# Optimization experiments

Measured on AMD Instinct MI355X. Metric: run time of the kernel, lower is better.

## Reference

```python
import jax, jax.numpy as jnp
import numpy as np

B, S, E, H = 4, 1024, 768, 8
HD = E // H
FF = 4 * E
SCALING = HD ** -0.5


def _layernorm(x, g, b, eps=1e-5):
    m = jnp.mean(x, axis=-1, keepdims=True)
    v = jnp.var(x, axis=-1, keepdims=True)
    return (x - m) / jnp.sqrt(v + eps) * g + b


def setup_inputs() -> dict:
    key = jax.random.key(0)
    ks = jax.random.split(key, 12)
    w = lambda k, shp: (jax.random.normal(k, shp, jnp.float32) * 0.02)
    return {
        "x": jax.random.normal(ks[0], (B, S, E), jnp.float32),
        "dist_map": jax.random.uniform(ks[1], (B, H, S, S), jnp.float32),
        "mask": jnp.zeros((B, S), jnp.int32),
        "Wq": w(ks[2], (E, E)), "bq": jnp.zeros((E,), jnp.float32),
        "Wk": w(ks[3], (E, E)), "bk": jnp.zeros((E,), jnp.float32),
        "Wv": w(ks[4], (E, E)), "bv": jnp.zeros((E,), jnp.float32),
        "Wo": w(ks[5], (E, E)), "bo": jnp.zeros((E,), jnp.float32),
        "ln1_g": jnp.ones((E,), jnp.float32), "ln1_b": jnp.zeros((E,), jnp.float32),
        "W1": w(ks[6], (FF, E)), "b1": jnp.zeros((FF,), jnp.float32),
        "W2": w(ks[7], (E, FF)), "b2": jnp.zeros((E,), jnp.float32),
        "ln2_g": jnp.ones((E,), jnp.float32), "ln2_b": jnp.zeros((E,), jnp.float32),
    }


def reference(x, dist_map, mask, Wq, bq, Wk, bk, Wv, bv, Wo, bo,
              ln1_g, ln1_b, W1, b1, W2, b2, ln2_g, ln2_b):
    # --- attention residual block (pre-norm) ---
    h = _layernorm(x, ln1_g, ln1_b)
    # NOTE: torch does .view(B, H, S, HD) directly on [B, S, E] -> pure reshape, no transpose
    q = (h @ Wq.T + bq).reshape(B, H, S, HD)
    k = (h @ Wk.T + bk).reshape(B, H, S, HD)
    v = (h @ Wv.T + bv).reshape(B, H, S, HD)
    attn_weights = jnp.einsum("bhqd,bhkd->bhqk", q, k)
    pad = mask.astype(bool)[:, None, None, :]          # [B,1,1,S]
    attn_weights = jnp.where(pad, -10000.0, attn_weights)  # mask BEFORE scaling (as in source)
    probs = jax.nn.softmax(attn_weights * SCALING, axis=-1)
    probs = (probs + dist_map) * 0.5                   # post-softmax dist bias
    ctx = jnp.einsum("bhal,bhlv->bhav", probs, v)      # [B,H,S,HD]
    ctx = ctx.transpose(0, 2, 1, 3).reshape(B, S, E)
    x1 = x + (ctx @ Wo.T + bo)
    # --- FFN residual block (pre-norm) ---
    h2 = _layernorm(x1, ln2_g, ln2_b)
    ffn = jax.nn.gelu(h2 @ W1.T + b1, approximate=False) @ W2.T + b2
    out = x1 + ffn
    return out, probs
```

## Files before the change

### kernel.cpp

```cpp
#include <hip/hip_runtime.h>
#include <math.h>

typedef unsigned short u16;
typedef u16   u16x8  __attribute__((ext_vector_type(8)));
typedef u16   u16x4  __attribute__((ext_vector_type(4)));
typedef __bf16 bf16x8 __attribute__((ext_vector_type(8)));
typedef float f32x4  __attribute__((ext_vector_type(4)));

#define SZ_BSE   3145728
#define HEADSZ   98304
#define SCALING  0.10206207261596577f

__device__ __forceinline__ u16 f2bf(float f) {
  union { float f; unsigned u; } c; c.f = f;
  unsigned u = c.u;
  return (u16)((u + 0x7fffu + ((u >> 16) & 1u)) >> 16);
}

typedef const __attribute__((address_space(1))) unsigned int* gas1_t;
typedef __attribute__((address_space(3))) unsigned int* las3_t;
__device__ __forceinline__ void gload16(const void* g, void* l) {
  __builtin_amdgcn_global_load_lds((gas1_t)g, (las3_t)l, 16, 0, 0);
}

__global__ __launch_bounds__(256) void cvt_k(const float* __restrict__ in,
                                             u16* __restrict__ out, int n) {
  int i = (blockIdx.x * 256 + threadIdx.x) * 4;
  if (i >= n) return;
  f32x4 v = *(const f32x4*)&in[i];
  u16x4 o; o[0]=f2bf(v[0]); o[1]=f2bf(v[1]); o[2]=f2bf(v[2]); o[3]=f2bf(v[3]);
  *(u16x4*)&out[i] = o;
}

__global__ __launch_bounds__(256) void ln_k(const float* __restrict__ x,
                                            const float* __restrict__ g,
                                            const float* __restrict__ b,
                                            u16* __restrict__ out) {
  const int row = blockIdx.x;
  const float* xr = x + (long)row * 768;
  const int t = threadIdx.x;
  float v0 = xr[t], v1 = xr[t + 256], v2 = xr[t + 512];
  float s = v0 + v1 + v2, ss = v0*v0 + v1*v1 + v2*v2;
  for (int o = 32; o > 0; o >>= 1) { s += __shfl_xor(s, o); ss += __shfl_xor(ss, o); }
  __shared__ float red[8];
  int w = t >> 6;
  if ((t & 63) == 0) { red[w] = s; red[w + 4] = ss; }
  __syncthreads();
  s  = red[0] + red[1] + red[2] + red[3];
  ss = red[4] + red[5] + red[6] + red[7];
  float mean = s * (1.0f / 768.0f);
  float var  = ss * (1.0f / 768.0f) - mean * mean;
  float rstd = rsqrtf(var + 1e-5f);
  u16* orow = out + (long)row * 768;
  orow[t]       = f2bf((v0 - mean) * rstd * g[t]       + b[t]);
  orow[t + 256] = f2bf((v1 - mean) * rstd * g[t + 256] + b[t + 256]);
  orow[t + 512] = f2bf((v2 - mean) * rstd * g[t + 512] + b[t + 512]);
}

__global__ __launch_bounds__(256) void vtrans_k(const u16* __restrict__ v,
                                                u16* __restrict__ vt) {
  __shared__ u16 tile[64 * 98];
  const int z = blockIdx.x >> 4;
  const int s0 = (blockIdx.x & 15) << 6;
  const int t = threadIdx.x;
  const u16* src = v + (long)z * HEADSZ + (long)s0 * 96;
#pragma unroll
  for (int it = 0; it < 3; ++it) {
    int i = it * 2048 + t * 8;
    int s = i / 96, d = i % 96;
    *(u16x8*)&tile[s * 98 + d] = *(const u16x8*)&src[i];
  }
  __syncthreads();
  u16* dst = vt + (long)z * HEADSZ + s0;
#pragma unroll
  for (int it = 0; it < 6; ++it) {
    int o = it * 1024 + t * 4;
    int d = o >> 6, s = o & 63;
    u16x4 wv;
#pragma unroll
    for (int j = 0; j < 4; ++j) wv[j] = tile[(s + j) * 98 + d];
    *(u16x4*)&dst[(long)d * 1024 + s] = wv;
  }
}

__global__ __launch_bounds__(256) void reduce_k(const float* __restrict__ p,
                                                const float* __restrict__ resid,
                                                const float* __restrict__ bias,
                                                float* __restrict__ out) {
  long i = ((long)blockIdx.x * 256 + threadIdx.x) * 4;
  f32x4 a = *(const f32x4*)&p[i];
  f32x4 b = *(const f32x4*)&p[3145728 + i];
  f32x4 c = *(const f32x4*)&p[6291456 + i];
  f32x4 r = *(const f32x4*)&resid[i];
  int cb = (int)(i % 768);
  f32x4 g = *(const f32x4*)&bias[cb];
  f32x4 o;
  o[0] = r[0] + g[0] + a[0] + b[0] + c[0];
  o[1] = r[1] + g[1] + a[1] + b[1] + c[1];
  o[2] = r[2] + g[2] + a[2] + b[2] + c[2];
  o[3] = r[3] + g[3] + a[3] + b[3] + c[3];
  *(f32x4*)&out[i] = o;
}

__global__ __launch_bounds__(256, 2)
void attn_k(const u16* __restrict__ qb, const u16* __restrict__ kb,
            const u16* __restrict__ vT, const float* __restrict__ dist,
            const int* __restrict__ maskp, float* __restrict__ probs,
            u16* __restrict__ ctx) {
  __shared__ u16 sP[64 * 88];
  __shared__ u16 sFlag[1024];

  const int t = threadIdx.x;
  const int z = blockIdx.y;
  const int r0 = blockIdx.x * 64;
  const int b = z >> 3, h = z & 7;

  {
    const int* mp = maskp + b * 1024 + t * 4;
    int4 mv = *(const int4*)mp;
    sFlag[t*4+0] = (u16)(mv.x != 0);
    sFlag[t*4+1] = (u16)(mv.y != 0);
    sFlag[t*4+2] = (u16)(mv.z != 0);
    sFlag[t*4+3] = (u16)(mv.w != 0);
  }
  __syncthreads();

  const int lane = t & 63;
  const int w = t >> 6;
  const int wr0 = w * 16;
  const int lr = lane & 15;
  const int lg = lane >> 4;

  const u16* qh = qb + (long)z * HEADSZ;
  const u16* kh = kb + (long)z * HEADSZ;
  const u16* vh = vT + (long)z * HEADSZ;
  const float* dh = dist + (long)z * 1048576;
  float* ph = probs + (long)z * 1048576;

  bf16x8 qa[3];
  {
    const u16* qr = qh + (long)(r0 + wr0 + lr) * 96 + lg * 8;
#pragma unroll
    for (int kf = 0; kf < 3; ++kf) qa[kf] = *(const bf16x8*)(qr + kf * 32);
  }

  const float neg = -10000.0f * SCALING;
  float srun[4] = {0.f, 0.f, 0.f, 0.f};

  for (int c = 0; c < 16; ++c) {
    const int c0 = c * 64;
    f32x4 a4[4] = {};
#pragma unroll
    for (int ni = 0; ni < 4; ++ni) {
      const u16* kr = kh + (long)(c0 + ni * 16 + lr) * 96 + lg * 8;
#pragma unroll
      for (int kf = 0; kf < 3; ++kf)
        a4[ni] = __builtin_amdgcn_mfma_f32_16x16x32_bf16(
            qa[kf], *(const bf16x8*)(kr + kf * 32), a4[ni], 0, 0, 0);
    }
#pragma unroll
    for (int ni = 0; ni < 4; ++ni) {
      bool fm = sFlag[c0 + ni * 16 + lr] != 0;
#pragma unroll
      for (int r = 0; r < 4; ++r) {
        float sv = fm ? neg : a4[ni][r] * SCALING;
        srun[r] += __expf(sv);
      }
    }
  }
  float inv[4];
#pragma unroll
  for (int r = 0; r < 4; ++r) {
    float s = srun[r];
    s += __shfl_xor(s, 1);
    s += __shfl_xor(s, 2);
    s += __shfl_xor(s, 4);
    s += __shfl_xor(s, 8);
    inv[r] = 1.0f / s;
  }

  f32x4 cacc[6] = {};
  for (int c = 0; c < 16; ++c) {
    const int c0 = c * 64;
    f32x4 dv[4];
#pragma unroll
    for (int ni = 0; ni < 4; ++ni) {
      const float* dp = dh + (long)(r0 + wr0 + lg * 4) * 1024 + c0 + ni * 16 + lr;
#pragma unroll
      for (int r = 0; r < 4; ++r) dv[ni][r] = dp[r * 1024];
    }
    f32x4 a4[4] = {};
#pragma unroll
    for (int ni = 0; ni < 4; ++ni) {
      const u16* kr = kh + (long)(c0 + ni * 16 + lr) * 96 + lg * 8;
#pragma unroll
      for (int kf = 0; kf < 3; ++kf)
        a4[ni] = __builtin_amdgcn_mfma_f32_16x16x32_bf16(
            qa[kf], *(const bf16x8*)(kr + kf * 32), a4[ni], 0, 0, 0);
    }
#pragma unroll
    for (int ni = 0; ni < 4; ++ni) {
      bool fm = sFlag[c0 + ni * 16 + lr] != 0;
      float* pp = ph + (long)(r0 + wr0 + lg * 4) * 1024 + c0 + ni * 16 + lr;
      int sb = (wr0 + lg * 4) * 88 + ni * 16 + lr;
#pragma unroll
      for (int r = 0; r < 4; ++r) {
        float sv = fm ? neg : a4[ni][r] * SCALING;
        float e = __expf(sv) * inv[r];
        float pr = (e + dv[ni][r]) * 0.5f;
        pp[r * 1024] = pr;
        sP[sb + r * 88] = f2bf(pr);
      }
    }
#pragma unroll
    for (int ks = 0; ks < 2; ++ks) {
      bf16x8 pa = *(const bf16x8*)&sP[(wr0 + lr) * 88 + ks * 32 + lg * 8];
      const u16* vr = vh + (long)lr * 1024 + c0 + ks * 32 + lg * 8;
#pragma unroll
      for (int n2 = 0; n2 < 6; ++n2) {
        bf16x8 vb = *(const bf16x8*)(vr + (long)n2 * 16 * 1024);
        cacc[n2] = __builtin_amdgcn_mfma_f32_16x16x32_bf16(pa, vb, cacc[n2], 0, 0, 0);
      }
    }
  }

  u16* cbase = ctx + (long)b * 786432 + h * 96;
#pragma unroll
  for (int n2 = 0; n2 < 6; ++n2) {
    int d = n2 * 16 + lr;
#pragma unroll
    for (int r = 0; r < 4; ++r)
      cbase[(long)(r0 + wr0 + lg * 4 + r) * 768 + d] = f2bf(cacc[n2][r]);
  }
}

enum { EPI_QKV = 0, EPI_GELU = 1, EPI_PARTIAL = 2 };

template <int EPI>
__global__ __launch_bounds__(256, 2)
void gemm_k(const u16* __restrict__ A, int lda,
            const u16* __restrict__ W, int ldw,
            void* __restrict__ Cv, long sCz, int ldc,
            const float* __restrict__ bias,
            int N, int K, int kchunks) {
  __shared__ u16 sA[4096];
  __shared__ u16 sB[4096];

  const int t  = threadIdx.x;
  const int kc = blockIdx.z;
  const int klen = K / kchunks;
  const int kbeg = kc * klen, kend = kbeg + klen;
  const int m0 = blockIdx.x * 128;
  const int n0 = blockIdx.y * 128;

  const int r0 = t >> 2;
  const int c0 = (t & 3) << 3;
  char* lA = (char*)sA + ((t >> 6) << 10);
  char* lB = (char*)sB + ((t >> 6) << 10);

  int bn0 = n0 + r0;      if (bn0 > N - 1) bn0 = N - 1;
  int bn1 = n0 + 64 + r0; if (bn1 > N - 1) bn1 = N - 1;
  const u16* gB0 = W + (long)bn0 * ldw + c0;
  const u16* gB1 = W + (long)bn1 * ldw + c0;
  const u16* gA0 = A + (long)(m0 + r0) * lda + c0;
  const u16* gA1 = gA0 + 64 * lda;

  const int lane = t & 63;
  const int w  = t >> 6;
  const int wm = (w >> 1) * 64, wn = (w & 1) * 64;
  const int lr = lane & 15, lg = lane >> 4;

  f32x4 acc[4][4] = {};

  for (int k0 = kbeg; k0 < kend; k0 += 32) {
    gload16(gA0 + k0, lA);
    gload16(gA1 + k0, lA + 4096);
    gload16(gB0 + k0, lB);
    gload16(gB1 + k0, lB + 4096);
    __syncthreads();

    bf16x8 aF[4], bF[4];
#pragma unroll
    for (int mi = 0; mi < 4; ++mi)
      aF[mi] = *(const bf16x8*)&sA[(wm + mi * 16 + lr) * 32 + lg * 8];
#pragma unroll
    for (int ni = 0; ni < 4; ++ni)
      bF[ni] = *(const bf16x8*)&sB[(wn + ni * 16 + lr) * 32 + lg * 8];
#pragma unroll
    for (int mi = 0; mi < 4; ++mi)
#pragma unroll
      for (int ni = 0; ni < 4; ++ni)
        acc[mi][ni] = __builtin_amdgcn_mfma_f32_16x16x32_bf16(aF[mi], bF[ni], acc[mi][ni], 0, 0, 0);
    __syncthreads();
  }

  long coff = (EPI == EPI_PARTIAL) ? (long)kc * sCz : 0;

#pragma unroll
  for (int mi = 0; mi < 4; ++mi) {
#pragma unroll
    for (int ni = 0; ni < 4; ++ni) {
      int gc = n0 + wn + ni * 16 + lr;
      if (gc >= N) continue;
      int gr0 = m0 + wm + mi * 16 + lg * 4;
#pragma unroll
      for (int r = 0; r < 4; ++r) {
        float vv = acc[mi][ni][r];
        if (EPI == EPI_QKV) {
          vv += bias[gc];
          int wsel = gc >= 1536 ? 2 : (gc >= 768 ? 1 : 0);
          int c = gc - wsel * 768;
          ((u16*)Cv)[(long)wsel * 3145728 + (long)(gr0 + r) * 768 + c] = f2bf(vv);
        } else if (EPI == EPI_GELU) {
          vv += bias[gc];
          vv = 0.5f * vv * (1.0f + erff(vv * 0.70710678118654752f));
          ((u16*)Cv)[coff + (long)(gr0 + r) * ldc + gc] = f2bf(vv);
        } else {
          ((float*)Cv)[coff + (long)(gr0 + r) * ldc + gc] = vv;
        }
      }
    }
  }
}

extern "C" void kernel_launch(void* const* d_in, const int* in_sizes, int n_in,
                              void* d_out, int out_size, void* d_ws, size_t ws_size,
                              hipStream_t stream) {
  (void)in_sizes; (void)n_in; (void)out_size; (void)ws_size;
  const float* x    = (const float*)d_in[0];
  const float* dist = (const float*)d_in[1];
  const int*   mask = (const int*)d_in[2];
  const float* Wq = (const float*)d_in[3];  const float* bq  = (const float*)d_in[4];
  const float* Wk = (const float*)d_in[5];  const float* bk  = (const float*)d_in[6];
  const float* Wv = (const float*)d_in[7];  const float* bv  = (const float*)d_in[8];
  const float* Wo = (const float*)d_in[9];  const float* bo  = (const float*)d_in[10];
  const float* g1 = (const float*)d_in[11]; const float* b1n = (const float*)d_in[12];
  const float* W1 = (const float*)d_in[13]; const float* b1f = (const float*)d_in[14];
  const float* W2 = (const float*)d_in[15]; const float* b2f = (const float*)d_in[16];
  const float* g2 = (const float*)d_in[17]; const float* b2n = (const float*)d_in[18];

  char* ws = (char*)d_ws;
  u16*   h    = (u16*)(ws + 0);
  u16*   ctx  = (u16*)(ws + 0);
  u16*   qkv  = (u16*)(ws + 6291456);
  u16*   q    = qkv;
  u16*   k    = (u16*)(ws + 12582912);
  u16*   v    = (u16*)(ws + 18874368);
  u16*   vT   = (u16*)(ws + 25165824);
  float* part = (float*)(ws + 6291456);
  u16*   h2   = (u16*)(ws + 31457280);
  u16*   ffn1 = (u16*)(ws + 44040192);
  float* x1   = (float*)(ws + 69206016);
  u16*   wqkvb= (u16*)(ws + 81788928);
  u16*   wob  = (u16*)(ws + 85327872);
  u16*   w1b  = (u16*)(ws + 86507520);
  u16*   w2b  = (u16*)(ws + 91226112);
  float* bqkv = (float*)(ws + 95944704);

  float* outp   = (float*)d_out;
  float* probs  = outp + SZ_BSE;

  cvt_k<<<576,  256, 0, stream>>>(Wq, wqkvb,           589824);
  cvt_k<<<576,  256, 0, stream>>>(Wk, wqkvb + 589824,  589824);
  cvt_k<<<576,  256, 0, stream>>>(Wv, wqkvb + 1179648, 589824);
  cvt_k<<<576,  256, 0, stream>>>(Wo, wob, 589824);
  cvt_k<<<2304, 256, 0, stream>>>(W1, w1b, 2359296);
  cvt_k<<<2304, 256, 0, stream>>>(W2, w2b, 2359296);
  hipMemcpyAsync(bqkv,        bq, 3072, hipMemcpyDeviceToDevice, stream);
  hipMemcpyAsync(bqkv + 768,  bk, 3072, hipMemcpyDeviceToDevice, stream);
  hipMemcpyAsync(bqkv + 1536, bv, 3072, hipMemcpyDeviceToDevice, stream);

  ln_k<<<4096, 256, 0, stream>>>(x, g1, b1n, h);

  gemm_k<EPI_QKV><<<dim3(32, 18, 1), 256, 0, stream>>>(
      h, 768, wqkvb, 768, qkv, 0, 768, bqkv, 2304, 768, 1);

  vtrans_k<<<512, 256, 0, stream>>>(v, vT);

  attn_k<<<dim3(16, 32), 256, 0, stream>>>(q, k, vT, dist, mask, probs, ctx);

  gemm_k<EPI_PARTIAL><<<dim3(32, 6, 3), 256, 0, stream>>>(
      ctx, 768, wob, 768, part, 3145728, 768, nullptr, 768, 768, 3);
  reduce_k<<<3072, 256, 0, stream>>>(part, x, bo, x1);

  ln_k<<<4096, 256, 0, stream>>>(x1, g2, b2n, h2);

  gemm_k<EPI_GELU><<<dim3(32, 24, 1), 256, 0, stream>>>(
      h2, 768, w1b, 768, ffn1, 0, 3072, b1f, 3072, 768, 1);

  gemm_k<EPI_PARTIAL><<<dim3(32, 6, 3), 256, 0, stream>>>(
      ffn1, 3072, w2b, 3072, part, 3145728, 768, nullptr, 768, 3072, 3);
  reduce_k<<<3072, 256, 0, stream>>>(part, x1, b2f, outp);
}
```

Before: 344.3 us.

## Split attention key range across two wave groups and vectorize probs/dist I/O

The attention kernel now launches 512 threads per block. Two groups of four waves each handle half of the 1024 keys: they combine their softmax row sums through shared memory and reduce the partial context accumulators through shared memory before writing. The dist_map read and probs write are restaged through a per-wave LDS tile, so each lane handles contiguous 16-float row segments with 128-bit loads and stores instead of strided scalar accesses. This adds parallelism and coalescing, at the cost of extra LDS traffic, extra barriers, and rounding exp to bf16 before the dist add, which slightly changes the precision of the probs output.

```diff
diff --git a/kernel.cpp b/kernel.cpp
--- a/kernel.cpp
+++ b/kernel.cpp
@@ -15,6 +15,9 @@
   union { float f; unsigned u; } c; c.f = f;
   unsigned u = c.u;
   return (u16)((u + 0x7fffu + ((u >> 16) & 1u)) >> 16);
+}
+__device__ __forceinline__ float bf2f(u16 v) {
+  union { unsigned u; float f; } c; c.u = ((unsigned)v) << 16; return c.f;
 }
 
 typedef const __attribute__((address_space(1))) unsigned int* gas1_t;
@@ -102,12 +105,14 @@
   *(f32x4*)&out[i] = o;
 }
 
-__global__ __launch_bounds__(256, 2)
+__global__ __launch_bounds__(512, 4)
 void attn_k(const u16* __restrict__ qb, const u16* __restrict__ kb,
             const u16* __restrict__ vT, const float* __restrict__ dist,
             const int* __restrict__ maskp, float* __restrict__ probs,
             u16* __restrict__ ctx) {
-  __shared__ u16 sP[64 * 88];
+  __shared__ u16 sP[8 * 16 * 72];
+  __shared__ float sX[4 * 64 * 24];
+  __shared__ float sSum[2][64];
   __shared__ u16 sFlag[1024];
 
   const int t = threadIdx.x;
@@ -116,20 +121,21 @@
   const int b = z >> 3, h = z & 7;
 
   {
-    const int* mp = maskp + b * 1024 + t * 4;
-    int4 mv = *(const int4*)mp;
-    sFlag[t*4+0] = (u16)(mv.x != 0);
-    sFlag[t*4+1] = (u16)(mv.y != 0);
-    sFlag[t*4+2] = (u16)(mv.z != 0);
-    sFlag[t*4+3] = (u16)(mv.w != 0);
+    const int* mp = maskp + b * 1024 + t * 2;
+    int2 mv = *(const int2*)mp;
+    sFlag[t * 2]     = (u16)(mv.x != 0);
+    sFlag[t * 2 + 1] = (u16)(mv.y != 0);
   }
   __syncthreads();
 
   const int lane = t & 63;
   const int w = t >> 6;
-  const int wr0 = w * 16;
+  const int rs = w & 3, ch = w >> 2;
+  const int wr0 = rs * 16;
   const int lr = lane & 15;
   const int lg = lane >> 4;
+  const int cbase = ch * 512;
+  u16* sPw = sP + w * (16 * 72);
 
   const u16* qh = qb + (long)z * HEADSZ;
   const u16* kh = kb + (long)z * HEADSZ;
@@ -147,8 +153,8 @@
   const float neg = -10000.0f * SCALING;
   float srun[4] = {0.f, 0.f, 0.f, 0.f};
 
-  for (int c = 0; c < 16; ++c) {
-    const int c0 = c * 64;
+  for (int c = 0; c < 8; ++c) {
+    const int c0 = cbase + c * 64;
     f32x4 a4[4] = {};
 #pragma unroll
     for (int ni = 0; ni < 4; ++ni) {
@@ -168,7 +174,6 @@
       }
     }
   }
-  float inv[4];
 #pragma unroll
   for (int r = 0; r < 4; ++r) {
     float s = srun[r];
@@ -176,19 +181,19 @@
     s += __shfl_xor(s, 2);
     s += __shfl_xor(s, 4);
     s += __shfl_xor(s, 8);
-    inv[r] = 1.0f / s;
-  }
-
+    if (lr == 0) sSum[ch][wr0 + lg * 4 + r] = s;
+  }
+  __syncthreads();
+  float inv[4];
+#pragma unroll
+  for (int r = 0; r < 4; ++r)
+    inv[r] = 1.0f / (sSum[0][wr0 + lg * 4 + r] + sSum[1][wr0 + lg * 4 + r]);
+
+  const int lrow = lane >> 2;
+  const int cg   = (lane & 3) * 16;
   f32x4 cacc[6] = {};
-  for (int c = 0; c < 16; ++c) {
-    const int c0 = c * 64;
-    f32x4 dv[4];
-#pragma unroll
-    for (int ni = 0; ni < 4; ++ni) {
-      const float* dp = dh + (long)(r0 + wr0 + lg * 4) * 1024 + c0 + ni * 16 + lr;
-#pragma unroll
-      for (int r = 0; r < 4; ++r) dv[ni][r] = dp[r * 1024];
-    }
+  for (int c = 0; c < 8; ++c) {
+    const int c0 = cbase + c * 64;
     f32x4 a4[4] = {};
 #pragma unroll
     for (int ni = 0; ni < 4; ++ni) {
@@ -201,20 +206,47 @@
 #pragma unroll
     for (int ni = 0; ni < 4; ++ni) {
       bool fm = sFlag[c0 + ni * 16 + lr] != 0;
-      float* pp = ph + (long)(r0 + wr0 + lg * 4) * 1024 + c0 + ni * 16 + lr;
-      int sb = (wr0 + lg * 4) * 88 + ni * 16 + lr;
 #pragma unroll
       for (int r = 0; r < 4; ++r) {
         float sv = fm ? neg : a4[ni][r] * SCALING;
-        float e = __expf(sv) * inv[r];
-        float pr = (e + dv[ni][r]) * 0.5f;
-        pp[r * 1024] = pr;
-        sP[sb + r * 88] = f2bf(pr);
-      }
+        sPw[(lg * 4 + r) * 72 + ni * 16 + lr] = f2bf(__expf(sv) * inv[r]);
+      }
+    }
+    {
+      u16x8 e0 = *(const u16x8*)&sPw[lrow * 72 + cg];
+      u16x8 e1 = *(const u16x8*)&sPw[lrow * 72 + cg + 8];
+      const float* dp = dh + (long)(r0 + wr0 + lrow) * 1024 + c0 + cg;
+      float* pp = ph + (long)(r0 + wr0 + lrow) * 1024 + c0 + cg;
+      f32x4 d0 = *(const f32x4*)dp;
+      f32x4 d1 = *(const f32x4*)(dp + 4);
+      f32x4 d2 = *(const f32x4*)(dp + 8);
+      f32x4 d3 = *(const f32x4*)(dp + 12);
+      f32x4 p0, p1, p2, p3;
+#pragma unroll
+      for (int j = 0; j < 4; ++j) {
+        p0[j] = (bf2f(e0[j])     + d0[j]) * 0.5f;
+        p1[j] = (bf2f(e0[4 + j]) + d1[j]) * 0.5f;
+        p2[j] = (bf2f(e1[j])     + d2[j]) * 0.5f;
+        p3[j] = (bf2f(e1[4 + j]) + d3[j]) * 0.5f;
+      }
+      *(f32x4*)pp        = p0;
+      *(f32x4*)(pp + 4)  = p1;
+      *(f32x4*)(pp + 8)  = p2;
+      *(f32x4*)(pp + 12) = p3;
+      u16x8 o0, o1;
+#pragma unroll
+      for (int j = 0; j < 4; ++j) {
+        o0[j]     = f2bf(p0[j]);
+        o0[4 + j] = f2bf(p1[j]);
+        o1[j]     = f2bf(p2[j]);
+        o1[4 + j] = f2bf(p3[j]);
+      }
+      *(u16x8*)&sPw[lrow * 72 + cg]     = o0;
+      *(u16x8*)&sPw[lrow * 72 + cg + 8] = o1;
     }
 #pragma unroll
     for (int ks = 0; ks < 2; ++ks) {
-      bf16x8 pa = *(const bf16x8*)&sP[(wr0 + lr) * 88 + ks * 32 + lg * 8];
+      bf16x8 pa = *(const bf16x8*)&sPw[lr * 72 + ks * 32 + lg * 8];
       const u16* vr = vh + (long)lr * 1024 + c0 + ks * 32 + lg * 8;
 #pragma unroll
       for (int n2 = 0; n2 < 6; ++n2) {
@@ -224,13 +256,24 @@
     }
   }
 
-  u16* cbase = ctx + (long)b * 786432 + h * 96;
-#pragma unroll
-  for (int n2 = 0; n2 < 6; ++n2) {
-    int d = n2 * 16 + lr;
-#pragma unroll
-    for (int r = 0; r < 4; ++r)
-      cbase[(long)(r0 + wr0 + lg * 4 + r) * 768 + d] = f2bf(cacc[n2][r]);
+  __syncthreads();
+  if (ch == 1) {
+    float* xp = sX + ((rs * 64 + lane) * 24);
+#pragma unroll
+    for (int n2 = 0; n2 < 6; ++n2) *(f32x4*)&xp[n2 * 4] = cacc[n2];
+  }
+  __syncthreads();
+  if (ch == 0) {
+    const float* xp = sX + ((rs * 64 + lane) * 24);
+    u16* cbp = ctx + (long)b * 786432 + h * 96;
+#pragma unroll
+    for (int n2 = 0; n2 < 6; ++n2) {
+      f32x4 xv = *(const f32x4*)&xp[n2 * 4];
+      int d = n2 * 16 + lr;
+#pragma unroll
+      for (int r = 0; r < 4; ++r)
+        cbp[(long)(r0 + wr0 + lg * 4 + r) * 768 + d] = f2bf(cacc[n2][r] + xv[r]);
+    }
   }
 }
 
@@ -377,7 +420,7 @@
 
   vtrans_k<<<512, 256, 0, stream>>>(v, vT);
 
-  attn_k<<<dim3(16, 32), 256, 0, stream>>>(q, k, vT, dist, mask, probs, ctx);
+  attn_k<<<dim3(16, 32), 512, 0, stream>>>(q, k, vT, dist, mask, probs, ctx);
 
   gemm_k<EPI_PARTIAL><<<dim3(32, 6, 3), 256, 0, stream>>>(
       ctx, 768, wob, 768, part, 3145728, 768, nullptr, 768, 768, 3);
```

Measured after the change: 332.5 us. 1.04x faster.
